# Performance work log

Measured on AMD Instinct MI355X. Metric: run time of the kernel, lower is better.

Reference implementation:

```python
import jax, jax.numpy as jnp
import numpy as np

LEBESGUE_P = 3          # lebesgue_p from __init__
WEIGHT_RANGE = 0.1      # weight init scale
B, C_IN, H, W = 32, 96, 56, 56
C_OUT, K = 384, 3
STRIDE = (1, 1)
PADDING = ((1, 1), (1, 1))


def setup_inputs() -> dict:
    key = jax.random.key(0)
    kx, kw = jax.random.split(key)
    x = jax.random.normal(kx, (B, C_IN, H, W), dtype=jnp.float32)
    # learned buffer 'weight': [out_channels, in_channels, kH, kW]
    weight = jax.random.normal(kw, (C_OUT, C_IN, K, K), dtype=jnp.float32) * WEIGHT_RANGE
    return {"x": x, "weight": weight}


def reference(x, weight):
    # get_pre_activations: conv with power-transformed weight sign(w)*|w|^(p-1)
    w_eff = jnp.sign(weight) * jnp.abs(weight) ** (LEBESGUE_P - 1)
    pre_x = jax.lax.conv_general_dilated(
        x, w_eff,
        window_strides=STRIDE,
        padding=PADDING,
        dimension_numbers=("NCHW", "OIHW", "NCHW"),
    )  # [B, C_OUT, H, W]

    # get_wta (groups=1): hard winner-take-all over channel dim per (b, h, w).
    # Original transposes/reshapes to [C_OUT, B*H*W], argmax over dim 0, one_hot,
    # then reshapes back; mathematically identical to a channel-axis argmax+one_hot.
    winners = jnp.argmax(pre_x, axis=1)                                   # [B, H, W]
    wta = jax.nn.one_hot(winners, pre_x.shape[1], axis=1, dtype=pre_x.dtype)  # [B, C_OUT, H, W]

    # forward(x, return_x_wta=True) returns (pre_x, wta); stack so output is one array
    return jnp.stack([pre_x, wta], axis=0)  # [2, B, C_OUT, H, W]
```

## Files before the change

### kernel.cpp

```cpp
#include <hip/hip_runtime.h>
#include <math.h>
#include <stdint.h>

#define CIN  96
#define COUT 384
#define HH   56
#define WW   56
#define BB   32

#define MARGIN   2e-3f
#define CAP      32000u
#define WT32_OFF (256 * 1024)
#define WT64_OFF (2 * 1024 * 1024)
#define WT16_OFF (5 * 1024 * 1024)
#define POSB     8

#define HL2      331776
#define XSB      6336

typedef _Float16 half8 __attribute__((ext_vector_type(8)));
typedef float    f32x4 __attribute__((ext_vector_type(4)));

__global__ void prep_wt16(const float* __restrict__ w, _Float16* __restrict__ wt16,
                          uint32_t* __restrict__ cnt) {
    int row = blockIdx.x * blockDim.x + threadIdx.x;
    if (row == 0) *cnt = 0u;
    if (row >= HL2 / 8) return;
    int c16 = row & 15;
    int rem = row >> 4;
    int khw = rem % 9;
    int rem2 = rem / 9;
    int kp  = rem2 % 12;
    int nb  = rem2 / 12;
    int co  = nb * 16 + c16;
    half8 hv, lv;
    #pragma unroll
    for (int j = 0; j < 8; ++j) {
        int ci = kp * 8 + j;
        float wv = w[(size_t)co * (CIN * 9) + ci * 9 + khw];
        double d = (double)wv;
        float ef = (float)(d * fabs(d));
        _Float16 hi = (_Float16)ef;
        hv[j] = hi;
        lv[j] = (_Float16)(ef - (float)hi);
    }
    *(half8*)(wt16 + (size_t)row * 8) = hv;
    *(half8*)(wt16 + HL2 + (size_t)row * 8) = lv;
}

__global__ void prep_wt64(const float* __restrict__ w, double* __restrict__ wt64) {
    int idx = blockIdx.x * blockDim.x + threadIdx.x;
    if (idx >= COUT * CIN * 9) return;
    int r  = idx / COUT;
    int co = idx - r * COUT;
    double d = (double)w[(size_t)co * (CIN * 9) + r];
    wt64[(size_t)r * COUT + co] = d * fabs(d);
}

__global__ void prep_tier2(const float* __restrict__ w, float* __restrict__ wt32,
                           double* __restrict__ wt64, uint32_t* __restrict__ cnt) {
    int idx = blockIdx.x * blockDim.x + threadIdx.x;
    if (idx == 0) *cnt = 0u;
    if (idx >= COUT * CIN * 9) return;
    int r  = idx / COUT;
    int co = idx - r * COUT;
    double d = (double)w[(size_t)co * (CIN * 9) + r];
    double e = d * fabs(d);
    wt64[(size_t)r * COUT + co] = e;
    wt32[(size_t)r * COUT + co] = (float)e;
}

__global__ __launch_bounds__(512, 4)
void conv_mfma(const float* __restrict__ x, const _Float16* __restrict__ wt16,
               float* __restrict__ out, uint32_t* __restrict__ cnt,
               uint32_t* __restrict__ flags) {
    const int h   = blockIdx.x;
    const int b   = blockIdx.y;
    const int tid = threadIdx.x;
    const int l   = tid & 63;
    const int wg  = tid >> 6;
    const int g   = l >> 4;
    const int c   = l & 15;

    __shared__ char lds[33792];
    _Float16* xs  = (_Float16*)lds;
    float*    T   = (float*)lds;
    float4*   red = (float4*)(lds + 25344);
    int*      win = (int*)(lds + 25344 + 8192);

    f32x4 acc[4][3];
    #pragma unroll
    for (int mf = 0; mf < 4; ++mf)
        #pragma unroll
        for (int nf = 0; nf < 3; ++nf)
            #pragma unroll
            for (int q = 0; q < 4; ++q) acc[mf][nf][q] = 0.0f;

    const _Float16* pa0 = xs + (g * 198 + c) * 8;

    auto stage = [&](int chunk) {
        _Float16* xsb = xs + (chunk & 1) * XSB;
        const int ci0 = chunk * 32;
        for (int idx = tid; idx < 4 * 198; idx += 512) {
            int cq  = idx / 198;
            int rem = idx - cq * 198;
            int r   = rem / 66;
            int col = rem - r * 66;
            int gh  = h + r - 1;
            int gw  = col - 1;
            half8 hv = {};
            if ((unsigned)gh < 56u && (unsigned)gw < 56u) {
                const float* px = x + (((size_t)b * CIN + (ci0 + cq * 8)) * HH + gh) * WW + gw;
                #pragma unroll
                for (int i = 0; i < 8; ++i) hv[i] = (_Float16)px[i * 3136];
            }
            *(half8*)(xsb + (size_t)(cq * 198 + rem) * 8) = hv;
        }
    };

    stage(0);
    __syncthreads();

    for (int chunk = 0; chunk < 3; ++chunk) {
        if (chunk < 2) stage(chunk + 1);

        const _Float16* pax = pa0 + (chunk & 1) * XSB;
        const _Float16* pb0 = wt16 + (size_t)(((wg * 3 + 0) * 12 + chunk * 4 + g) * 9) * 128 + c * 8;
        const _Float16* pb1 = wt16 + (size_t)(((wg * 3 + 1) * 12 + chunk * 4 + g) * 9) * 128 + c * 8;
        const _Float16* pb2 = wt16 + (size_t)(((wg * 3 + 2) * 12 + chunk * 4 + g) * 9) * 128 + c * 8;

        half8 B0 = *(const half8*)(pb0);
        half8 B1 = *(const half8*)(pb1);
        half8 B2 = *(const half8*)(pb2);

        #pragma unroll
        for (int khw = 0; khw < 9; ++khw) {
            const int kh = khw / 3;
            const int kw = khw - kh * 3;
            half8 Bn0, Bn1, Bn2;
            if (khw < 8) {
                Bn0 = *(const half8*)(pb0 + (khw + 1) * 128);
                Bn1 = *(const half8*)(pb1 + (khw + 1) * 128);
                Bn2 = *(const half8*)(pb2 + (khw + 1) * 128);
            }
            #pragma unroll
            for (int mf = 0; mf < 4; ++mf) {
                half8 Ah = *(const half8*)(pax + (kh * 66 + mf * 16 + kw) * 8);
                acc[mf][0] = __builtin_amdgcn_mfma_f32_16x16x32_f16(Ah, B0, acc[mf][0], 0, 0, 0);
                acc[mf][1] = __builtin_amdgcn_mfma_f32_16x16x32_f16(Ah, B1, acc[mf][1], 0, 0, 0);
                acc[mf][2] = __builtin_amdgcn_mfma_f32_16x16x32_f16(Ah, B2, acc[mf][2], 0, 0, 0);
            }
            if (khw < 8) { B0 = Bn0; B1 = Bn1; B2 = Bn2; }
        }
        __syncthreads();
    }

    #pragma unroll
    for (int mf = 0; mf < 4; ++mf) {
        #pragma unroll
        for (int q = 0; q < 4; ++q) {
            float best = acc[mf][0][q];
            int   bco  = wg * 48 + c;
            float sec  = -1e30f;
            #pragma unroll
            for (int nf = 1; nf < 3; ++nf) {
                float v = acc[mf][nf][q];
                if (v > best) { sec = best; best = v; bco = wg * 48 + nf * 16 + c; }
                else if (v > sec) sec = v;
            }
            #pragma unroll
            for (int off = 1; off <= 8; off <<= 1) {
                float ov = __shfl_xor(best, off, 64);
                int   oc = __shfl_xor(bco,  off, 64);
                float os = __shfl_xor(sec,  off, 64);
                if (ov > best || (ov == best && oc < bco)) {
                    sec = fmaxf(best, os);
                    best = ov; bco = oc;
                } else {
                    sec = fmaxf(sec, ov);
                }
            }
            if (c == 0) {
                int m = mf * 16 + g * 4 + q;
                red[wg * 64 + m] = make_float4(best, sec, __int_as_float(bco), 0.0f);
            }
        }
    }
    __syncthreads();
    {
        const int m = tid >> 3;
        const int j = tid & 7;
        float4 v = red[j * 64 + m];
        float best = v.x, sec = v.y;
        int   bco  = __float_as_int(v.z);
        #pragma unroll
        for (int off = 1; off <= 4; off <<= 1) {
            float ov = __shfl_xor(best, off, 64);
            int   oc = __shfl_xor(bco,  off, 64);
            float os = __shfl_xor(sec,  off, 64);
            if (ov > best || (ov == best && oc < bco)) {
                sec = fmaxf(best, os);
                best = ov; bco = oc;
            } else {
                sec = fmaxf(sec, ov);
            }
        }
        if (j == 0 && m < 56) {
            win[m] = bco;
            if ((best - sec) < MARGIN) {
                uint32_t k = atomicAdd(cnt, 1u);
                if (k < CAP) flags[k] = (uint32_t)((b * 56 + h) * 56 + m);
            }
        }
    }
    __syncthreads();

    const size_t wta_off = (size_t)BB * COUT * HH * WW;
    for (int rnd = 0; rnd < 4; ++rnd) {
        if ((wg >> 1) == rnd) {
            const int wq = wg & 1;
            #pragma unroll
            for (int mf = 0; mf < 4; ++mf)
                #pragma unroll
                for (int nf = 0; nf < 3; ++nf)
                    #pragma unroll
                    for (int q = 0; q < 4; ++q)
                        T[(wq * 48 + nf * 16 + c) * 65 + mf * 16 + g * 4 + q] = acc[mf][nf][q];
        }
        __syncthreads();
        for (int t = tid; t < 96 * 64; t += 512) {
            int co_l = t >> 6;
            int m    = t & 63;
            if (m < 56) {
                int co  = rnd * 96 + co_l;
                float v = T[co_l * 65 + m];
                size_t o = ((size_t)(b * COUT + co)) * 3136 + (size_t)h * 56 + m;
                out[o] = v;
                out[wta_off + o] = (co == win[m]) ? 1.0f : 0.0f;
            }
        }
        __syncthreads();
    }
}

__global__ __launch_bounds__(512, 2)
void conv_wta_f32(const float* __restrict__ x, const float* __restrict__ wt,
                  float* __restrict__ out, uint32_t* __restrict__ cnt,
                  uint32_t* __restrict__ flags) {
    const int h0  = blockIdx.x * 2;
    const int b   = blockIdx.y;
    const int tid = threadIdx.x;
    const int cg  = tid & 63;
    const int wg  = tid >> 6;
    const int co0 = cg * 6;
    const int ws0 = wg * 7;

    __shared__ float xs[32 * 4 * 58];
    __shared__ int   win[2][56];

    float acc[2][6][7];
    #pragma unroll
    for (int r = 0; r < 2; ++r)
        #pragma unroll
        for (int c = 0; c < 6; ++c)
            #pragma unroll
            for (int i = 0; i < 7; ++i) acc[r][c][i] = 0.0f;

    for (int chunk = 0; chunk < 3; ++chunk) {
        const int ci0 = chunk * 32;
        __syncthreads();
        for (int idx = tid; idx < 32 * 4 * 58; idx += 512) {
            int ci  = idx / 232;
            int rem = idx - ci * 232;
            int r   = rem / 58;
            int c   = rem - r * 58;
            int gh  = h0 + r - 1;
            int gw  = c - 1;
            float v = 0.0f;
            if ((unsigned)gh < 56u && (unsigned)gw < 56u)
                v = x[(((size_t)b * CIN + (ci0 + ci)) * HH + gh) * WW + gw];
            xs[idx] = v;
        }
        __syncthreads();
        for (int ci = 0; ci < 32; ++ci) {
            const int gci = ci0 + ci;
            #pragma unroll
            for (int kh = 0; kh < 3; ++kh) {
                float xa[9], xb[9];
                const float* xr0 = &xs[(ci * 4 + kh) * 58 + ws0];
                const float* xr1 = &xs[(ci * 4 + kh + 1) * 58 + ws0];
                #pragma unroll
                for (int j = 0; j < 9; ++j) { xa[j] = xr0[j]; xb[j] = xr1[j]; }
                #pragma unroll
                for (int kw = 0; kw < 3; ++kw) {
                    const float* p = wt + (size_t)((gci * 3 + kh) * 3 + kw) * COUT + co0;
                    float2 w01 = *(const float2*)(p);
                    float2 w23 = *(const float2*)(p + 2);
                    float2 w45 = *(const float2*)(p + 4);
                    float wd[6] = {w01.x, w01.y, w23.x, w23.y, w45.x, w45.y};
                    #pragma unroll
                    for (int c = 0; c < 6; ++c)
                        #pragma unroll
                        for (int i = 0; i < 7; ++i) {
                            acc[0][c][i] = fmaf(wd[c], xa[i + kw], acc[0][c][i]);
                            acc[1][c][i] = fmaf(wd[c], xb[i + kw], acc[1][c][i]);
                        }
                }
            }
        }
    }

    #pragma unroll
    for (int rr = 0; rr < 2; ++rr) {
        #pragma unroll
        for (int i = 0; i < 7; ++i) {
            float best = acc[rr][0][i];
            int   bco  = co0;
            float sec  = -1e30f;
            #pragma unroll
            for (int c = 1; c < 6; ++c) {
                float v = acc[rr][c][i];
                if (v > best) { sec = best; best = v; bco = co0 + c; }
                else if (v > sec) sec = v;
            }
            #pragma unroll
            for (int off = 32; off > 0; off >>= 1) {
                float ov = __shfl_xor(best, off, 64);
                int   oc = __shfl_xor(bco,  off, 64);
                float os = __shfl_xor(sec,  off, 64);
                if (ov > best || (ov == best && oc < bco)) {
                    sec = fmaxf(best, os);
                    best = ov; bco = oc;
                } else {
                    sec = fmaxf(sec, ov);
                }
            }
            if (cg == 0) {
                win[rr][ws0 + i] = bco;
                if ((best - sec) < MARGIN) {
                    uint32_t k = atomicAdd(cnt, 1u);
                    if (k < CAP) flags[k] = (uint32_t)((b * 56 + (h0 + rr)) * 56 + (ws0 + i));
                }
            }
        }
    }

    const size_t wta_off = (size_t)BB * COUT * HH * WW;
    float* ldsT = xs;
    __syncthreads();
    for (int k = 0; k < 8; ++k) {
        if ((cg >> 3) == k) {
            const int cr = (cg & 7) * 6;
            #pragma unroll
            for (int c = 0; c < 6; ++c)
                #pragma unroll
                for (int rr = 0; rr < 2; ++rr)
                    #pragma unroll
                    for (int i = 0; i < 7; ++i)
                        ldsT[(cr + c) * 113 + rr * 56 + ws0 + i] = acc[rr][c][i];
        }
        __syncthreads();
        for (int l = tid; l < 48 * 112; l += 512) {
            int co_r = l / 112;
            int rem  = l - co_r * 112;
            int rr   = rem / 56;
            int w    = rem - rr * 56;
            int co   = k * 48 + co_r;
            float v  = ldsT[co_r * 113 + rem];
            size_t o = ((size_t)(b * COUT + co)) * 3136 + (size_t)(h0 + rr) * 56 + w;
            out[o] = v;
            out[wta_off + o] = (co == win[rr][w]) ? 1.0f : 0.0f;
        }
        __syncthreads();
    }
}

__global__ __launch_bounds__(384)
void fixup_f64(const float* __restrict__ x, const double* __restrict__ wt64,
               float* __restrict__ out, const uint32_t* __restrict__ cnt,
               const uint32_t* __restrict__ flags) {
    __shared__ float  xp[POSB][CIN * 9];
    __shared__ double sv[POSB][COUT];
    __shared__ int winners[POSB];

    uint32_t n = *cnt;
    if (n > CAP) n = CAP;
    const int tid = threadIdx.x;
    const int wg  = tid >> 6;
    const int lane = tid & 63;
    const size_t wta_off = (size_t)BB * COUT * HH * WW;

    for (uint32_t base = blockIdx.x * POSB; base < n; base += gridDim.x * POSB) {
        int np = (int)(n - base) < POSB ? (int)(n - base) : POSB;
        __syncthreads();
        for (int idx = tid; idx < np * CIN * 9; idx += 384) {
            int p  = idx / (CIN * 9);
            int r  = idx - p * (CIN * 9);
            int ci = r / 9;
            int k  = r - ci * 9;
            int kh = k / 3, kw = k - kh * 3;
            uint32_t pos = flags[base + p];
            int w_ = pos % 56;
            int h_ = (pos / 56) % 56;
            int b_ = pos / 3136;
            int gh = h_ + kh - 1, gw = w_ + kw - 1;
            float v = 0.0f;
            if ((unsigned)gh < 56u && (unsigned)gw < 56u)
                v = x[(((size_t)b_ * CIN + ci) * HH + gh) * WW + gw];
            xp[p][r] = v;
        }
        __syncthreads();
        {
            const int co = tid;
            double a[POSB];
            #pragma unroll
            for (int p = 0; p < POSB; ++p) a[p] = 0.0;
            #pragma unroll 4
            for (int r = 0; r < CIN * 9; ++r) {
                double wd = wt64[(size_t)r * COUT + co];
                #pragma unroll
                for (int p = 0; p < POSB; ++p)
                    a[p] = fma(wd, (double)xp[p][r], a[p]);
            }
            #pragma unroll
            for (int p = 0; p < POSB; ++p) sv[p][co] = a[p];
        }
        __syncthreads();
        for (int p = wg; p < np; p += 6) {
            double best = sv[p][lane * 6];
            int bco = lane * 6;
            #pragma unroll
            for (int c = 1; c < 6; ++c) {
                double v2 = sv[p][lane * 6 + c];
                if (v2 > best) { best = v2; bco = lane * 6 + c; }
            }
            #pragma unroll
            for (int off = 32; off > 0; off >>= 1) {
                double ov = __shfl_xor(best, off, 64);
                int    oc = __shfl_xor(bco,  off, 64);
                if (ov > best || (ov == best && oc < bco)) { best = ov; bco = oc; }
            }
            if (lane == 0) winners[p] = bco;
        }
        __syncthreads();
        for (int idx = tid; idx < np * COUT; idx += 384) {
            int p  = idx / COUT;
            int co = idx - p * COUT;
            uint32_t pos = flags[base + p];
            int w_ = pos % 56;
            int h_ = (pos / 56) % 56;
            int b_ = pos / 3136;
            size_t o = (((size_t)b_ * COUT + co) * HH + h_) * WW + w_;
            out[o] = (float)sv[p][co];
            out[wta_off + o] = (co == winners[p]) ? 1.0f : 0.0f;
        }
        __syncthreads();
    }
}

__global__ __launch_bounds__(256, 2)
void conv_wta_f64(const float* __restrict__ x, const float* __restrict__ wraw,
                  float* __restrict__ out) {
    const int whalf = blockIdx.x;
    const int h     = blockIdx.y;
    const int b     = blockIdx.z;
    const int tid   = threadIdx.x;
    const int cg    = tid & 63;
    const int wg    = tid >> 6;
    const int co0   = cg * 6;
    const int wbase = whalf * 28 + wg * 7;

    __shared__ float xs[32 * 3 * 30];
    double acc[6][7];
    #pragma unroll
    for (int c = 0; c < 6; ++c)
        #pragma unroll
        for (int i = 0; i < 7; ++i) acc[c][i] = 0.0;

    for (int chunk = 0; chunk < 3; ++chunk) {
        const int ci0 = chunk * 32;
        __syncthreads();
        for (int idx = tid; idx < 32 * 3 * 30; idx += 256) {
            int ci = idx / 90, rem = idx - ci * 90;
            int r = rem / 30, c = rem - r * 30;
            int gh = h + r - 1, gw = whalf * 28 - 1 + c;
            float v = 0.0f;
            if ((unsigned)gh < 56u && (unsigned)gw < 56u)
                v = x[(((size_t)b * CIN + (ci0 + ci)) * HH + gh) * WW + gw];
            xs[idx] = v;
        }
        __syncthreads();
        for (int ci = 0; ci < 32; ++ci) {
            const int gci = ci0 + ci;
            #pragma unroll
            for (int kh = 0; kh < 3; ++kh) {
                double xd[9];
                #pragma unroll
                for (int j = 0; j < 9; ++j)
                    xd[j] = (double)xs[(ci * 3 + kh) * 30 + wg * 7 + j];
                #pragma unroll
                for (int kw = 0; kw < 3; ++kw) {
                    #pragma unroll
                    for (int c = 0; c < 6; ++c) {
                        double d = (double)wraw[(size_t)(co0 + c) * (CIN * 9) + gci * 9 + kh * 3 + kw];
                        double wd = d * fabs(d);
                        #pragma unroll
                        for (int i = 0; i < 7; ++i)
                            acc[c][i] = fma(wd, xd[i + kw], acc[c][i]);
                    }
                }
            }
        }
    }
    const size_t wta_off = (size_t)BB * COUT * HH * WW;
    #pragma unroll
    for (int i = 0; i < 7; ++i) {
        double best = acc[0][i];
        int bco = co0;
        #pragma unroll
        for (int c = 1; c < 6; ++c)
            if (acc[c][i] > best) { best = acc[c][i]; bco = co0 + c; }
        #pragma unroll
        for (int off = 32; off > 0; off >>= 1) {
            double ov = __shfl_xor(best, off, 64);
            int    oc = __shfl_xor(bco,  off, 64);
            if (ov > best || (ov == best && oc < bco)) { best = ov; bco = oc; }
        }
        const int w = wbase + i;
        #pragma unroll
        for (int c = 0; c < 6; ++c) {
            size_t o = (((size_t)b * COUT + (co0 + c)) * HH + h) * WW + w;
            out[o] = (float)acc[c][i];
            out[wta_off + o] = (co0 + c == bco) ? 1.0f : 0.0f;
        }
    }
}

extern "C" void kernel_launch(void* const* d_in, const int* in_sizes, int n_in,
                              void* d_out, int out_size, void* d_ws, size_t ws_size,
                              hipStream_t stream) {
    (void)in_sizes; (void)n_in; (void)out_size;
    const float* x = (const float*)d_in[0];
    const float* w = (const float*)d_in[1];
    float* out = (float*)d_out;

    const size_t need16 = (size_t)WT16_OFF + (size_t)2 * HL2 * sizeof(_Float16);
    const size_t need64 = (size_t)WT64_OFF + (size_t)COUT * CIN * 9 * sizeof(double);

    uint32_t* cnt   = (uint32_t*)d_ws;
    uint32_t* flags = (uint32_t*)((char*)d_ws + 256);
    float*    wt32  = (float*)((char*)d_ws + WT32_OFF);
    double*   wt64  = (double*)((char*)d_ws + WT64_OFF);
    _Float16* wt16  = (_Float16*)((char*)d_ws + WT16_OFF);

    if (ws_size >= need16) {
        prep_wt16<<<(HL2 / 8 + 255) / 256, 256, 0, stream>>>(w, wt16, cnt);
        prep_wt64<<<(COUT * CIN * 9 + 255) / 256, 256, 0, stream>>>(w, wt64);
        conv_mfma<<<dim3(56, 32), 512, 0, stream>>>(x, wt16, out, cnt, flags);
        fixup_f64<<<256, 384, 0, stream>>>(x, wt64, out, cnt, flags);
    } else if (ws_size >= need64) {
        prep_tier2<<<(COUT * CIN * 9 + 255) / 256, 256, 0, stream>>>(w, wt32, wt64, cnt);
        conv_wta_f32<<<dim3(28, 32), 512, 0, stream>>>(x, wt32, out, cnt, flags);
        fixup_f64<<<256, 384, 0, stream>>>(x, wt64, out, cnt, flags);
    } else {
        conv_wta_f64<<<dim3(2, 56, 32), 256, 0, stream>>>(x, w, out);
    }
}
```

Baseline: 331.8 us.

## Split conv_mfma output channels across 12 waves instead of 8

```diff
diff --git a/kernel.cpp b/kernel.cpp
--- a/kernel.cpp
+++ b/kernel.cpp
@@ -70,7 +70,7 @@
     wt32[(size_t)r * COUT + co] = (float)e;
 }
 
-__global__ __launch_bounds__(512, 4)
+__global__ __launch_bounds__(768, 6)
 void conv_mfma(const float* __restrict__ x, const _Float16* __restrict__ wt16,
                float* __restrict__ out, uint32_t* __restrict__ cnt,
                uint32_t* __restrict__ flags) {
@@ -82,17 +82,17 @@
     const int g   = l >> 4;
     const int c   = l & 15;
 
-    __shared__ char lds[33792];
+    __shared__ char lds[37888];
     _Float16* xs  = (_Float16*)lds;
     float*    T   = (float*)lds;
     float4*   red = (float4*)(lds + 25344);
-    int*      win = (int*)(lds + 25344 + 8192);
-
-    f32x4 acc[4][3];
+    int*      win = (int*)(lds + 25344 + 12288);
+
+    f32x4 acc[4][2];
     #pragma unroll
     for (int mf = 0; mf < 4; ++mf)
         #pragma unroll
-        for (int nf = 0; nf < 3; ++nf)
+        for (int nf = 0; nf < 2; ++nf)
             #pragma unroll
             for (int q = 0; q < 4; ++q) acc[mf][nf][q] = 0.0f;
 
@@ -101,7 +101,7 @@
     auto stage = [&](int chunk) {
         _Float16* xsb = xs + (chunk & 1) * XSB;
         const int ci0 = chunk * 32;
-        for (int idx = tid; idx < 4 * 198; idx += 512) {
+        for (int idx = tid; idx < 4 * 198; idx += 768) {
             int cq  = idx / 198;
             int rem = idx - cq * 198;
             int r   = rem / 66;
@@ -125,32 +125,21 @@
         if (chunk < 2) stage(chunk + 1);
 
         const _Float16* pax = pa0 + (chunk & 1) * XSB;
-        const _Float16* pb0 = wt16 + (size_t)(((wg * 3 + 0) * 12 + chunk * 4 + g) * 9) * 128 + c * 8;
-        const _Float16* pb1 = wt16 + (size_t)(((wg * 3 + 1) * 12 + chunk * 4 + g) * 9) * 128 + c * 8;
-        const _Float16* pb2 = wt16 + (size_t)(((wg * 3 + 2) * 12 + chunk * 4 + g) * 9) * 128 + c * 8;
-
-        half8 B0 = *(const half8*)(pb0);
-        half8 B1 = *(const half8*)(pb1);
-        half8 B2 = *(const half8*)(pb2);
+        const _Float16* pb0 = wt16 + (size_t)(((wg * 2 + 0) * 12 + chunk * 4 + g) * 9) * 128 + c * 8;
+        const _Float16* pb1 = wt16 + (size_t)(((wg * 2 + 1) * 12 + chunk * 4 + g) * 9) * 128 + c * 8;
 
         #pragma unroll
         for (int khw = 0; khw < 9; ++khw) {
             const int kh = khw / 3;
             const int kw = khw - kh * 3;
-            half8 Bn0, Bn1, Bn2;
-            if (khw < 8) {
-                Bn0 = *(const half8*)(pb0 + (khw + 1) * 128);
-                Bn1 = *(const half8*)(pb1 + (khw + 1) * 128);
-                Bn2 = *(const half8*)(pb2 + (khw + 1) * 128);
-            }
+            half8 B0 = *(const half8*)(pb0 + khw * 128);
+            half8 B1 = *(const half8*)(pb1 + khw * 128);
             #pragma unroll
             for (int mf = 0; mf < 4; ++mf) {
                 half8 Ah = *(const half8*)(pax + (kh * 66 + mf * 16 + kw) * 8);
                 acc[mf][0] = __builtin_amdgcn_mfma_f32_16x16x32_f16(Ah, B0, acc[mf][0], 0, 0, 0);
                 acc[mf][1] = __builtin_amdgcn_mfma_f32_16x16x32_f16(Ah, B1, acc[mf][1], 0, 0, 0);
-                acc[mf][2] = __builtin_amdgcn_mfma_f32_16x16x32_f16(Ah, B2, acc[mf][2], 0, 0, 0);
-            }
-            if (khw < 8) { B0 = Bn0; B1 = Bn1; B2 = Bn2; }
+            }
         }
         __syncthreads();
     }
@@ -160,13 +149,12 @@
         #pragma unroll
         for (int q = 0; q < 4; ++q) {
             float best = acc[mf][0][q];
-            int   bco  = wg * 48 + c;
+            int   bco  = wg * 32 + c;
             float sec  = -1e30f;
-            #pragma unroll
-            for (int nf = 1; nf < 3; ++nf) {
-                float v = acc[mf][nf][q];
-                if (v > best) { sec = best; best = v; bco = wg * 48 + nf * 16 + c; }
-                else if (v > sec) sec = v;
+            {
+                float v = acc[mf][1][q];
+                if (v > best) { sec = best; best = v; bco = wg * 32 + 16 + c; }
+                else sec = v;
             }
             #pragma unroll
             for (int off = 1; off <= 8; off <<= 1) {
@@ -190,26 +178,37 @@
     {
         const int m = tid >> 3;
         const int j = tid & 7;
-        float4 v = red[j * 64 + m];
-        float best = v.x, sec = v.y;
-        int   bco  = __float_as_int(v.z);
-        #pragma unroll
-        for (int off = 1; off <= 4; off <<= 1) {
-            float ov = __shfl_xor(best, off, 64);
-            int   oc = __shfl_xor(bco,  off, 64);
-            float os = __shfl_xor(sec,  off, 64);
-            if (ov > best || (ov == best && oc < bco)) {
-                sec = fmaxf(best, os);
-                best = ov; bco = oc;
-            } else {
-                sec = fmaxf(sec, ov);
-            }
-        }
-        if (j == 0 && m < 56) {
-            win[m] = bco;
-            if ((best - sec) < MARGIN) {
-                uint32_t k = atomicAdd(cnt, 1u);
-                if (k < CAP) flags[k] = (uint32_t)((b * 56 + h) * 56 + m);
+        if (m < 64) {
+            float4 a = red[j * 64 + m];
+            float best = a.x, sec = a.y;
+            int   bco  = __float_as_int(a.z);
+            if (j < 4) {
+                float4 d = red[(j + 8) * 64 + m];
+                if (d.x > best) {
+                    sec = fmaxf(best, d.y);
+                    best = d.x; bco = __float_as_int(d.z);
+                } else {
+                    sec = fmaxf(sec, d.x);
+                }
+            }
+            #pragma unroll
+            for (int off = 1; off <= 4; off <<= 1) {
+                float ov = __shfl_xor(best, off, 64);
+                int   oc = __shfl_xor(bco,  off, 64);
+                float os = __shfl_xor(sec,  off, 64);
+                if (ov > best || (ov == best && oc < bco)) {
+                    sec = fmaxf(best, os);
+                    best = ov; bco = oc;
+                } else {
+                    sec = fmaxf(sec, ov);
+                }
+            }
+            if (j == 0 && m < 56) {
+                win[m] = bco;
+                if ((best - sec) < MARGIN) {
+                    uint32_t k = atomicAdd(cnt, 1u);
+                    if (k < CAP) flags[k] = (uint32_t)((b * 56 + h) * 56 + m);
+                }
             }
         }
     }
@@ -217,18 +216,18 @@
 
     const size_t wta_off = (size_t)BB * COUT * HH * WW;
     for (int rnd = 0; rnd < 4; ++rnd) {
-        if ((wg >> 1) == rnd) {
-            const int wq = wg & 1;
+        if (wg / 3 == rnd) {
+            const int wq = wg % 3;
             #pragma unroll
             for (int mf = 0; mf < 4; ++mf)
                 #pragma unroll
-                for (int nf = 0; nf < 3; ++nf)
+                for (int nf = 0; nf < 2; ++nf)
                     #pragma unroll
                     for (int q = 0; q < 4; ++q)
-                        T[(wq * 48 + nf * 16 + c) * 65 + mf * 16 + g * 4 + q] = acc[mf][nf][q];
-        }
-        __syncthreads();
-        for (int t = tid; t < 96 * 64; t += 512) {
+                        T[(wq * 32 + nf * 16 + c) * 65 + mf * 16 + g * 4 + q] = acc[mf][nf][q];
+        }
+        __syncthreads();
+        for (int t = tid; t < 96 * 64; t += 768) {
             int co_l = t >> 6;
             int m    = t & 63;
             if (m < 56) {
@@ -556,7 +555,7 @@
     if (ws_size >= need16) {
         prep_wt16<<<(HL2 / 8 + 255) / 256, 256, 0, stream>>>(w, wt16, cnt);
         prep_wt64<<<(COUT * CIN * 9 + 255) / 256, 256, 0, stream>>>(w, wt64);
-        conv_mfma<<<dim3(56, 32), 512, 0, stream>>>(x, wt16, out, cnt, flags);
+        conv_mfma<<<dim3(56, 32), 768, 0, stream>>>(x, wt16, out, cnt, flags);
         fixup_f64<<<256, 384, 0, stream>>>(x, wt64, out, cnt, flags);
     } else if (ws_size >= need64) {
         prep_tier2<<<(COUT * CIN * 9 + 255) / 256, 256, 0, stream>>>(w, wt32, wt64, cnt);
```

New measurement: 337.0 us. Within noise of the previous version (+1.6%).
